# Optimization experiments

Hardware: AMD Instinct MI355X
Metric: run time of the kernel (lower is better)

## Reference

```python
import jax, jax.numpy as jnp
import numpy as np
import math

WIN = 7
N = WIN * WIN            # 49 tokens per window
DIM = 192
HEADS = 6
HEAD_DIM = DIM // HEADS  # 32
B_ = 4096                # batch * num_windows
NUM_WIN = 64             # windows per image (mask leading dim)
TABLE = (2 * WIN - 1) ** 2  # 169


def _rel_pos_index(wh, ww):
    coords = np.stack(np.meshgrid(np.arange(wh), np.arange(ww), indexing='ij'))  # [2,wh,ww]
    cf = coords.reshape(2, -1)                       # [2, N]
    rc = (cf[:, :, None] - cf[:, None, :]).transpose(1, 2, 0).astype(np.int32)  # [N,N,2]
    rc[:, :, 0] += wh - 1
    rc[:, :, 1] += ww - 1
    rc[:, :, 0] *= 2 * ww - 1
    return rc.sum(-1)                                # [N,N] in [0, TABLE)


def setup_inputs() -> dict:
    key = jax.random.key(0)
    ks = jax.random.split(key, 6)
    x = jax.random.normal(ks[0], (B_, N, DIM), dtype=jnp.float32)
    # shifted-window style 0/-100 mask
    m = jax.random.uniform(ks[1], (NUM_WIN, N, N))
    mask = jnp.where(m < 0.8, 0.0, -100.0).astype(jnp.float32)
    qkv_w = jax.random.normal(ks[2], (3 * DIM, DIM), dtype=jnp.float32) * 0.02
    qkv_b = jnp.zeros((3 * DIM,), dtype=jnp.float32)
    logit_scale = jnp.full((HEADS, 1, 1), math.log(10.0), dtype=jnp.float32)
    rel_bias_table = jax.random.normal(ks[3], (TABLE, HEADS), dtype=jnp.float32) * 0.02
    rel_index = jnp.asarray(_rel_pos_index(WIN, WIN), dtype=jnp.int32)
    proj_w = jax.random.normal(ks[4], (DIM, DIM), dtype=jnp.float32) * 0.02
    proj_b = jnp.zeros((DIM,), dtype=jnp.float32)
    return {"x": x, "mask": mask, "qkv_w": qkv_w, "qkv_b": qkv_b,
            "logit_scale": logit_scale, "rel_bias_table": rel_bias_table,
            "rel_index": rel_index, "proj_w": proj_w, "proj_b": proj_b}


def reference(x, mask, qkv_w, qkv_b, logit_scale, rel_bias_table, rel_index, proj_w, proj_b):
    B, n, C = x.shape
    H = logit_scale.shape[0]
    qkv = (jnp.einsum('bnc,oc->bno', x, qkv_w) + qkv_b).reshape(B, n, 3, H, -1)
    qkv = jnp.transpose(qkv, (2, 0, 3, 1, 4))  # [3,B,H,n,hd]
    q, k, v = qkv[0], qkv[1], qkv[2]
    # cosine attention: l2-normalize q and k (torch F.normalize, eps=1e-12)
    qn = q / jnp.maximum(jnp.linalg.norm(q, axis=-1, keepdims=True), 1e-12)
    kn = k / jnp.maximum(jnp.linalg.norm(k, axis=-1, keepdims=True), 1e-12)
    attn = jnp.einsum('bhnd,bhmd->bhnm', qn, kn)
    scale = jnp.exp(jnp.minimum(logit_scale, math.log(1.0 / 0.01)))  # [H,1,1]
    attn = attn * scale
    # gathered relative position bias -> [1,H,n,n]
    bias = rel_bias_table[rel_index.reshape(-1)].reshape(n, n, H)
    attn = attn + jnp.transpose(bias, (2, 0, 1))[None]
    nw = mask.shape[0]
    attn = attn.reshape(B // nw, nw, H, n, n) + mask[None, :, None]
    attn = jax.nn.softmax(attn.reshape(B, H, n, n), axis=-1)
    out = jnp.einsum('bhnm,bhmd->bhnd', attn, v)
    out = jnp.transpose(out, (0, 2, 1, 3)).reshape(B, n, -1)
    return jnp.einsum('bnc,oc->bno', out, proj_w) + proj_b
```

## Files before the change

kernel.cpp:

```cpp
#include <hip/hip_runtime.h>
#include <hip/hip_fp16.h>


#define NTOK 49
#define DIM 192
#define NH 6
#define BATCH 4096
#define MTOT 200704

typedef __attribute__((ext_vector_type(4))) float f32x4;
typedef __attribute__((ext_vector_type(8))) _Float16 f16x8;
typedef __attribute__((ext_vector_type(4))) _Float16 f16x4h;
typedef __attribute__((ext_vector_type(2))) _Float16 f16x2h;

#define W1_OFF 0
#define W2_OFF 221184
#define BMI_OFF 294912
#define HSC_OFF 2260992
#define Q_OFF 4194304
#define K_OFF 81264640
#define V_OFF 158334976

#define LOG2E 1.44269504088896f
#define SM_SHIFT 16.0f

#define MFMA16(a, b, c) __builtin_amdgcn_mfma_f32_16x16x32_f16(a, b, c, 0, 0, 0)

#if __has_builtin(__builtin_amdgcn_fdot2)
__device__ __forceinline__ float dot8(const f16x8 v, float acc) {
#pragma unroll
  for (int e = 0; e < 4; ++e) {
    f16x2h p = {v[2 * e], v[2 * e + 1]};
    acc = __builtin_amdgcn_fdot2(p, p, acc, false);
  }
  return acc;
}
#else
__device__ __forceinline__ float dot8(const f16x8 v, float acc) {
#pragma unroll
  for (int e = 0; e < 8; ++e) acc += (float)v[e] * (float)v[e];
  return acc;
}
#endif

#define GLOAD_LDS16(gsrc, ldst)                                      \
  __builtin_amdgcn_global_load_lds(                                  \
      (const __attribute__((address_space(1))) unsigned int*)(gsrc), \
      (__attribute__((address_space(3))) unsigned int*)(ldst), 16, 0, 0)

__global__ __launch_bounds__(256) void k_setup(
    const float* __restrict__ qkv_w, const float* __restrict__ proj_w,
    const float* __restrict__ mask, const float* __restrict__ table,
    const int* __restrict__ rel_index, const float* __restrict__ ls,
    char* __restrict__ W1s, _Float16* __restrict__ W2,
    _Float16* __restrict__ bmi, float* __restrict__ hsc) {
  int idx = blockIdx.x * 256 + threadIdx.x;
  if (idx < 576 * 192) {
    int col = idx / 192, kk = idx - col * 192;
    unsigned int o = (unsigned int)(col & 31) * 384 + (unsigned int)kk * 2;
    unsigned int d = (unsigned int)(col >> 5) * 12288 +
                     (o ^ (((unsigned int)col & 7) << 4));
    *(_Float16*)(W1s + d) = (_Float16)qkv_w[idx];
  }
  if (idx < 192 * 192) W2[idx] = (_Float16)proj_w[idx];
  if (idx < NH) hsc[idx] = __expf(fminf(ls[idx], 4.60517019f)) * LOG2E;
  if (idx < 64 * NH * 2401) {
    int p = idx / 2401, rem = idx % 2401;
    int i = rem / 49, j = rem % 49;
    int wdx = p / NH, h = p % NH;
    bmi[(size_t)p * 2548 + i * 52 + j] =
        (_Float16)((table[rel_index[i * 49 + j] * NH + h] +
                    mask[wdx * 2401 + i * 49 + j]) * LOG2E);
  }
}

__global__ __launch_bounds__(256, 2) void k_qkv(
    const float* __restrict__ x, const char* __restrict__ W1s,
    const float* __restrict__ qkv_b, _Float16* __restrict__ q16,
    _Float16* __restrict__ k16, _Float16* __restrict__ v16) {
  __shared__ __align__(16) char wlds[2][24576];

  const int tid = threadIdx.x;
  const int lane = tid & 63;
  const int w = tid >> 6;
  const int rowbase = blockIdx.x * 256 + w * 64;
  const int L = lane & 15;
  const int g = lane >> 4;

  f16x8 ax[4][6];
#pragma unroll
  for (int rt = 0; rt < 4; ++rt) {
    const float* xr = x + (size_t)(rowbase + rt * 16 + L) * DIM + 8 * g;
#pragma unroll
    for (int kf = 0; kf < 6; ++kf) {
      f32x4 lo = *(const f32x4*)(xr + 32 * kf);
      f32x4 hi = *(const f32x4*)(xr + 32 * kf + 4);
      f16x8 v;
      v[0] = (_Float16)lo[0]; v[1] = (_Float16)lo[1];
      v[2] = (_Float16)lo[2]; v[3] = (_Float16)lo[3];
      v[4] = (_Float16)hi[0]; v[5] = (_Float16)hi[1];
      v[6] = (_Float16)hi[2]; v[7] = (_Float16)hi[3];
      ax[rt][kf] = v;
    }
  }
  int qkb[4];
#pragma unroll
  for (int rt = 0; rt < 4; ++rt) {
    int row = rowbase + rt * 16 + L;
    int bb = row / 49, n = row - bb * 49;
    qkb[rt] = bb * 9408 + n * 32;
  }

#pragma unroll
  for (int r = 0; r < 6; ++r)
    GLOAD_LDS16(W1s + (w * 6 + r) * 1024 + lane * 16,
                &wlds[0][(w * 6 + r) * 1024]);

#pragma unroll 1
  for (int grp = 0; grp < 9; ++grp) {
    __syncthreads();
    const int cur = grp & 1;

    if (grp < 8) {
#pragma unroll
      for (int r = 0; r < 6; ++r)
        GLOAD_LDS16(W1s + (size_t)(grp + 1) * 24576 + (w * 6 + r) * 1024 +
                        lane * 16,
                    &wlds[cur ^ 1][(w * 6 + r) * 1024]);
    }

    const unsigned int sw = (unsigned int)(L & 7) << 4;
#pragma unroll
    for (int tl = 0; tl < 2; ++tl) {
      const int t = grp * 2 + tl;
      const int s = t / 6;
      const int tt = t - 6 * s;
      _Float16* dst = (s == 0) ? q16 : (s == 1) ? k16 : v16;
      const char* base = &wlds[cur][tl * 12288];
#pragma unroll
      for (int ct = 0; ct < 2; ++ct) {
        f16x8 wf[6];
#pragma unroll
        for (int kf = 0; kf < 6; ++kf) {
          unsigned int o0 = (unsigned int)(16 * ct + L) * 384 +
                            (unsigned int)kf * 64 + (unsigned int)g * 16;
          wf[kf] = *(const f16x8*)(base + (o0 ^ sw));
        }
        f32x4 acc[4];
#pragma unroll
        for (int rt = 0; rt < 4; ++rt) acc[rt] = (f32x4){0.f, 0.f, 0.f, 0.f};
#pragma unroll
        for (int kf = 0; kf < 6; ++kf)
#pragma unroll
          for (int rt = 0; rt < 4; ++rt)
            acc[rt] = MFMA16(wf[kf], ax[rt][kf], acc[rt]);
        const f32x4 bv =
            *(const f32x4*)(qkv_b + 192 * s + 32 * tt + 16 * ct + 4 * g);
        const int off = tt * 1568 + 16 * ct + 4 * g;
#pragma unroll
        for (int rt = 0; rt < 4; ++rt) {
          f16x4h pk;
#pragma unroll
          for (int r = 0; r < 4; ++r) pk[r] = (_Float16)(acc[rt][r] + bv[r]);
          *(f16x4h*)(dst + qkb[rt] + off) = pk;
        }
      }
    }
  }
}

__global__ __launch_bounds__(768, 6) void k_attn2(
    const _Float16* __restrict__ q16, const _Float16* __restrict__ k16,
    const _Float16* __restrict__ v16, const _Float16* __restrict__ bmi,
    const float* __restrict__ hsc, const _Float16* __restrict__ W2,
    const float* __restrict__ proj_b, float* __restrict__ out) {
  __shared__ __align__(128) _Float16 pl[12][1024];
  __shared__ __align__(16) _Float16 ao[2][64 * 200];

  const int tid = threadIdx.x;
  const int wv = tid >> 6;
  const int ww = wv / 6;
  const int h = wv - 6 * ww;
  const int b = blockIdx.x * 2 + ww;
  const int lane = tid & 63;
  const int L = lane & 15;
  const int g = lane >> 4;

  const size_t qoff = ((size_t)b * NH + h) * 1568;
  const float hs = hsc[h];

  f16x8 vf[2][2];
#pragma unroll
  for (int dt = 0; dt < 2; ++dt)
#pragma unroll
    for (int kf = 0; kf < 2; ++kf)
#pragma unroll
      for (int e = 0; e < 8; ++e) {
        int j = 32 * kf + 8 * g + e;
        if (j > 48) j = 48;
        vf[dt][kf][e] = v16[qoff + j * 32 + 16 * dt + L];
      }

  f16x8 kf4[4];
#pragma unroll
  for (int jt = 0; jt < 4; ++jt) {
    int jrow = 16 * jt + L; if (jrow > 48) jrow = 48;
    kf4[jt] = *(const f16x8*)(k16 + qoff + jrow * 32 + 8 * g);
    float kk = dot8(kf4[jt], 0.f);
    kk += __shfl_xor(kk, 16);
    kk += __shfl_xor(kk, 32);
    const float inv = rsqrtf(fmaxf(kk, 1e-24f));
#pragma unroll
    for (int e = 0; e < 8; ++e)
      kf4[jt][e] = (_Float16)((float)kf4[jt][e] * inv);
  }

  char* plw = (char*)&pl[wv][0];
  const unsigned int pswz =
      (((unsigned int)L & 1) << 6) | (((unsigned int)L & 12) << 2);
  const _Float16* bmp = bmi + ((size_t)(b & 63) * NH + h) * 2548;

#pragma unroll 1
  for (int it = 0; it < 4; ++it) {
    int irow = 16 * it + L; if (irow > 48) irow = 48;
    f16x8 qf = *(const f16x8*)(q16 + qoff + irow * 32 + 8 * g);
    float qq = dot8(qf, 0.f);
    qq += __shfl_xor(qq, 16);
    qq += __shfl_xor(qq, 32);
    const float qr = rsqrtf(fmaxf(qq, 1e-24f)) * hs;

    f32x4 st[4];
#pragma unroll
    for (int jt = 0; jt < 4; ++jt) {
      f32x4 z = {0.f, 0.f, 0.f, 0.f};
      st[jt] = MFMA16(kf4[jt], qf, z);
    }
    const _Float16* bp = bmp + (16 * it + L) * 52 + 4 * g;
    float sum = 0.f;
#pragma unroll
    for (int jt = 0; jt < 4; ++jt) {
      f16x4h bm4 = *(const f16x4h*)(bp + 16 * jt);
#pragma unroll
      for (int r = 0; r < 4; ++r) {
        int j = 16 * jt + 4 * g + r;
        float v = (j < NTOK)
                      ? exp2f(fmaf(st[jt][r], qr, (float)bm4[r]) - SM_SHIFT)
                      : 0.0f;
        st[jt][r] = v;
        sum += v;
      }
    }
    sum += __shfl_xor(sum, 16);
    sum += __shfl_xor(sum, 32);
    const float is = 1.0f / sum;

#pragma unroll
    for (int jt = 0; jt < 4; ++jt) {
      f16x4h pk;
#pragma unroll
      for (int r = 0; r < 4; ++r) pk[r] = (_Float16)(st[jt][r] * is);
      *(f16x4h*)(plw +
                 (((unsigned int)L * 128 + 32u * jt + 8u * g) ^ pswz)) = pk;
    }
    f16x8 pa0 =
        *(const f16x8*)(plw + (((unsigned int)L * 128 + 16u * g) ^ pswz));
    f16x8 pa1 = *(const f16x8*)(plw +
                                (((unsigned int)L * 128 + 64 + 16u * g) ^ pswz));
#pragma unroll
    for (int dt = 0; dt < 2; ++dt) {
      f32x4 o4 = {0.f, 0.f, 0.f, 0.f};
      o4 = MFMA16(vf[dt][0], pa0, o4);
      o4 = MFMA16(vf[dt][1], pa1, o4);
      f16x4h ok;
#pragma unroll
      for (int r = 0; r < 4; ++r) ok[r] = (_Float16)o4[r];
      *(f16x4h*)(&ao[ww][(16 * it + L) * 200 + 32 * h + 16 * dt + 4 * g]) = ok;
    }
  }
  __syncthreads();

#pragma unroll
  for (int cp = 0; cp < 2; ++cp) {
    const int ct = h + 6 * cp;
    const _Float16* wp = W2 + (size_t)(16 * ct + L) * DIM + 8 * g;
    f16x8 wfr[6];
#pragma unroll
    for (int kf = 0; kf < 6; ++kf) wfr[kf] = *(const f16x8*)(wp + 32 * kf);
    const f32x4 pbv = *(const f32x4*)(proj_b + 16 * ct + 4 * g);
#pragma unroll 1
    for (int mt = 0; mt < 4; ++mt) {
      f32x4 acc = {0.f, 0.f, 0.f, 0.f};
#pragma unroll
      for (int kf = 0; kf < 6; ++kf) {
        f16x8 af =
            *(const f16x8*)(&ao[ww][(16 * mt + L) * 200 + 32 * kf + 8 * g]);
        acc = MFMA16(wfr[kf], af, acc);
      }
      const int row = 16 * mt + L;
      if (row < NTOK) {
        f32x4 o;
#pragma unroll
        for (int r = 0; r < 4; ++r) o[r] = acc[r] + pbv[r];
        *(f32x4*)(&out[((size_t)b * NTOK + row) * DIM + 16 * ct + 4 * g]) = o;
      }
    }
  }
}

extern "C" void kernel_launch(void* const* d_in, const int* in_sizes, int n_in,
                              void* d_out, int out_size, void* d_ws, size_t ws_size,
                              hipStream_t stream) {
  const float* x     = (const float*)d_in[0];
  const float* mask  = (const float*)d_in[1];
  const float* qkv_w = (const float*)d_in[2];
  const float* qkv_b = (const float*)d_in[3];
  const float* ls    = (const float*)d_in[4];
  const float* tbl   = (const float*)d_in[5];
  const int*   ridx  = (const int*)d_in[6];
  const float* pw    = (const float*)d_in[7];
  const float* pb    = (const float*)d_in[8];
  float* out = (float*)d_out;
  char* ws = (char*)d_ws;

  char* W1s = ws + W1_OFF;
  _Float16* W2 = (_Float16*)(ws + W2_OFF);
  _Float16* bmi = (_Float16*)(ws + BMI_OFF);
  float* hsc = (float*)(ws + HSC_OFF);
  _Float16* q16 = (_Float16*)(ws + Q_OFF);
  _Float16* k16 = (_Float16*)(ws + K_OFF);
  _Float16* v16 = (_Float16*)(ws + V_OFF);

  hipLaunchKernelGGL(k_setup, dim3(3602), dim3(256), 0, stream,
                     qkv_w, pw, mask, tbl, ridx, ls, W1s, W2, bmi, hsc);
  hipLaunchKernelGGL(k_qkv, dim3(MTOT / 256), dim3(256), 0, stream,
                     x, W1s, qkv_b, q16, k16, v16);
  hipLaunchKernelGGL(k_attn2, dim3(BATCH / 2), dim3(768), 0, stream,
                     q16, k16, v16, bmi, hsc, W2, pb, out);
}
```

Baseline: 252.8 us.

## Fuse q/k L2-normalization and logit scale into QKV projection epilogue

Moves the cosine-attention normalization of q and k, plus the per-head logit scale on q, out of the attention kernel and into the QKV GEMM epilogue, computed in fp32 before the fp16 store. The attention kernel no longer does dot products, shuffles and rescaling of K fragments per wave or q rows per iteration. The QKV kernel also halves rows per block (128 instead of 256), launches twice as many blocks, and raises the occupancy hint to 3. In exchange each block reloads the full weight matrix for half as many rows, which doubles weight traffic from L2 into LDS. Storing scaled q in fp16 also changes rounding, since the logit scale can reach 100.

```diff
diff --git a/kernel.cpp b/kernel.cpp
--- a/kernel.cpp
+++ b/kernel.cpp
@@ -11,7 +11,6 @@
 typedef __attribute__((ext_vector_type(4))) float f32x4;
 typedef __attribute__((ext_vector_type(8))) _Float16 f16x8;
 typedef __attribute__((ext_vector_type(4))) _Float16 f16x4h;
-typedef __attribute__((ext_vector_type(2))) _Float16 f16x2h;
 
 #define W1_OFF 0
 #define W2_OFF 221184
@@ -25,23 +24,6 @@
 #define SM_SHIFT 16.0f
 
 #define MFMA16(a, b, c) __builtin_amdgcn_mfma_f32_16x16x32_f16(a, b, c, 0, 0, 0)
-
-#if __has_builtin(__builtin_amdgcn_fdot2)
-__device__ __forceinline__ float dot8(const f16x8 v, float acc) {
-#pragma unroll
-  for (int e = 0; e < 4; ++e) {
-    f16x2h p = {v[2 * e], v[2 * e + 1]};
-    acc = __builtin_amdgcn_fdot2(p, p, acc, false);
-  }
-  return acc;
-}
-#else
-__device__ __forceinline__ float dot8(const f16x8 v, float acc) {
-#pragma unroll
-  for (int e = 0; e < 8; ++e) acc += (float)v[e] * (float)v[e];
-  return acc;
-}
-#endif
 
 #define GLOAD_LDS16(gsrc, ldst)                                      \
   __builtin_amdgcn_global_load_lds(                                  \
@@ -74,22 +56,23 @@
   }
 }
 
-__global__ __launch_bounds__(256, 2) void k_qkv(
+__global__ __launch_bounds__(256, 3) void k_qkv(
     const float* __restrict__ x, const char* __restrict__ W1s,
-    const float* __restrict__ qkv_b, _Float16* __restrict__ q16,
-    _Float16* __restrict__ k16, _Float16* __restrict__ v16) {
+    const float* __restrict__ qkv_b, const float* __restrict__ hsc,
+    _Float16* __restrict__ q16, _Float16* __restrict__ k16,
+    _Float16* __restrict__ v16) {
   __shared__ __align__(16) char wlds[2][24576];
 
   const int tid = threadIdx.x;
   const int lane = tid & 63;
   const int w = tid >> 6;
-  const int rowbase = blockIdx.x * 256 + w * 64;
+  const int rowbase = blockIdx.x * 128 + w * 32;
   const int L = lane & 15;
   const int g = lane >> 4;
 
-  f16x8 ax[4][6];
-#pragma unroll
-  for (int rt = 0; rt < 4; ++rt) {
+  f16x8 ax[2][6];
+#pragma unroll
+  for (int rt = 0; rt < 2; ++rt) {
     const float* xr = x + (size_t)(rowbase + rt * 16 + L) * DIM + 8 * g;
 #pragma unroll
     for (int kf = 0; kf < 6; ++kf) {
@@ -103,9 +86,9 @@
       ax[rt][kf] = v;
     }
   }
-  int qkb[4];
-#pragma unroll
-  for (int rt = 0; rt < 4; ++rt) {
+  int qkb[2];
+#pragma unroll
+  for (int rt = 0; rt < 2; ++rt) {
     int row = rowbase + rt * 16 + L;
     int bb = row / 49, n = row - bb * 49;
     qkb[rt] = bb * 9408 + n * 32;
@@ -137,6 +120,7 @@
       const int tt = t - 6 * s;
       _Float16* dst = (s == 0) ? q16 : (s == 1) ? k16 : v16;
       const char* base = &wlds[cur][tl * 12288];
+      f32x4 av[2][2];
 #pragma unroll
       for (int ct = 0; ct < 2; ++ct) {
         f16x8 wf[6];
@@ -146,22 +130,47 @@
                             (unsigned int)kf * 64 + (unsigned int)g * 16;
           wf[kf] = *(const f16x8*)(base + (o0 ^ sw));
         }
-        f32x4 acc[4];
-#pragma unroll
-        for (int rt = 0; rt < 4; ++rt) acc[rt] = (f32x4){0.f, 0.f, 0.f, 0.f};
-#pragma unroll
-        for (int kf = 0; kf < 6; ++kf)
-#pragma unroll
-          for (int rt = 0; rt < 4; ++rt)
-            acc[rt] = MFMA16(wf[kf], ax[rt][kf], acc[rt]);
+        f32x4 a0 = {0.f, 0.f, 0.f, 0.f}, a1 = {0.f, 0.f, 0.f, 0.f};
+#pragma unroll
+        for (int kf = 0; kf < 6; ++kf) {
+          a0 = MFMA16(wf[kf], ax[0][kf], a0);
+          a1 = MFMA16(wf[kf], ax[1][kf], a1);
+        }
         const f32x4 bv =
             *(const f32x4*)(qkv_b + 192 * s + 32 * tt + 16 * ct + 4 * g);
+#pragma unroll
+        for (int r = 0; r < 4; ++r) {
+          av[ct][0][r] = a0[r] + bv[r];
+          av[ct][1][r] = a1[r] + bv[r];
+        }
+      }
+      float sc[2] = {1.f, 1.f};
+      if (s < 2) {
+#pragma unroll
+        for (int rt = 0; rt < 2; ++rt) {
+          float ss = 0.f;
+#pragma unroll
+          for (int ct = 0; ct < 2; ++ct)
+#pragma unroll
+            for (int r = 0; r < 4; ++r) ss += av[ct][rt][r] * av[ct][rt][r];
+          ss += __shfl_xor(ss, 16);
+          ss += __shfl_xor(ss, 32);
+          sc[rt] = rsqrtf(fmaxf(ss, 1e-24f));
+        }
+        if (s == 0) {
+          const float hs = hsc[tt];
+          sc[0] *= hs; sc[1] *= hs;
+        }
+      }
+#pragma unroll
+      for (int ct = 0; ct < 2; ++ct) {
         const int off = tt * 1568 + 16 * ct + 4 * g;
 #pragma unroll
-        for (int rt = 0; rt < 4; ++rt) {
+        for (int rt = 0; rt < 2; ++rt) {
           f16x4h pk;
 #pragma unroll
-          for (int r = 0; r < 4; ++r) pk[r] = (_Float16)(acc[rt][r] + bv[r]);
+          for (int r = 0; r < 4; ++r)
+            pk[r] = (_Float16)(av[ct][rt][r] * sc[rt]);
           *(f16x4h*)(dst + qkb[rt] + off) = pk;
         }
       }
@@ -172,8 +181,8 @@
 __global__ __launch_bounds__(768, 6) void k_attn2(
     const _Float16* __restrict__ q16, const _Float16* __restrict__ k16,
     const _Float16* __restrict__ v16, const _Float16* __restrict__ bmi,
-    const float* __restrict__ hsc, const _Float16* __restrict__ W2,
-    const float* __restrict__ proj_b, float* __restrict__ out) {
+    const _Float16* __restrict__ W2, const float* __restrict__ proj_b,
+    float* __restrict__ out) {
   __shared__ __align__(128) _Float16 pl[12][1024];
   __shared__ __align__(16) _Float16 ao[2][64 * 200];
 
@@ -187,7 +196,6 @@
   const int g = lane >> 4;
 
   const size_t qoff = ((size_t)b * NH + h) * 1568;
-  const float hs = hsc[h];
 
   f16x8 vf[2][2];
 #pragma unroll
@@ -206,13 +214,6 @@
   for (int jt = 0; jt < 4; ++jt) {
     int jrow = 16 * jt + L; if (jrow > 48) jrow = 48;
     kf4[jt] = *(const f16x8*)(k16 + qoff + jrow * 32 + 8 * g);
-    float kk = dot8(kf4[jt], 0.f);
-    kk += __shfl_xor(kk, 16);
-    kk += __shfl_xor(kk, 32);
-    const float inv = rsqrtf(fmaxf(kk, 1e-24f));
-#pragma unroll
-    for (int e = 0; e < 8; ++e)
-      kf4[jt][e] = (_Float16)((float)kf4[jt][e] * inv);
   }
 
   char* plw = (char*)&pl[wv][0];
@@ -224,10 +225,6 @@
   for (int it = 0; it < 4; ++it) {
     int irow = 16 * it + L; if (irow > 48) irow = 48;
     f16x8 qf = *(const f16x8*)(q16 + qoff + irow * 32 + 8 * g);
-    float qq = dot8(qf, 0.f);
-    qq += __shfl_xor(qq, 16);
-    qq += __shfl_xor(qq, 32);
-    const float qr = rsqrtf(fmaxf(qq, 1e-24f)) * hs;
 
     f32x4 st[4];
 #pragma unroll
@@ -244,7 +241,7 @@
       for (int r = 0; r < 4; ++r) {
         int j = 16 * jt + 4 * g + r;
         float v = (j < NTOK)
-                      ? exp2f(fmaf(st[jt][r], qr, (float)bm4[r]) - SM_SHIFT)
+                      ? exp2f(st[jt][r] + (float)bm4[r] - SM_SHIFT)
                       : 0.0f;
         st[jt][r] = v;
         sum += v;
@@ -332,8 +329,8 @@
 
   hipLaunchKernelGGL(k_setup, dim3(3602), dim3(256), 0, stream,
                      qkv_w, pw, mask, tbl, ridx, ls, W1s, W2, bmi, hsc);
-  hipLaunchKernelGGL(k_qkv, dim3(MTOT / 256), dim3(256), 0, stream,
-                     x, W1s, qkv_b, q16, k16, v16);
+  hipLaunchKernelGGL(k_qkv, dim3(MTOT / 128), dim3(256), 0, stream,
+                     x, W1s, qkv_b, hsc, q16, k16, v16);
   hipLaunchKernelGGL(k_attn2, dim3(BATCH / 2), dim3(768), 0, stream,
-                     q16, k16, v16, bmi, hsc, W2, pb, out);
+                     q16, k16, v16, bmi, W2, pb, out);
 }
```

After: 241.2 us. 4.6% less time.
